# Optimization experiments

Hardware: AMD Instinct MI355X
Metric: run time of the kernel (lower is better)

## Reference

```python
import jax, jax.numpy as jnp
import numpy as np

GRAPH_SIZE = 100000  # == N, used as scalar multiplier on Q


def setup_inputs() -> dict:
    key = jax.random.key(0)
    ks = jax.random.split(key, 10)
    N, D, K, C, S = 100000, 128, 10, 50000, 100
    inp = {
        "seeds_idx_pad": jax.random.randint(ks[0], (1, S), 0, N + 1),  # N = pad row
        "seeds_idx_num": jnp.full((1, 1), 50.0, dtype=jnp.float32),
        "candidates_idx": jax.random.randint(ks[1], (C,), 0, N),
        "all_nodes": jnp.arange(N),
        "mask": jnp.ones((N, 1), dtype=jnp.float32),
        "features": jax.random.normal(ks[2], (N, D), dtype=jnp.float32),
        "neigh_idx": jax.random.randint(ks[3], (N, K), 0, N),
        "W_self": jax.random.normal(ks[4], (D, D), dtype=jnp.float32) * 0.05,
        "W_neigh": jax.random.normal(ks[5], (D, D), dtype=jnp.float32) * 0.05,
        "W1": jax.random.normal(ks[6], (D, D + 1), dtype=jnp.float32) * 0.05,
        "W2": jax.random.normal(ks[7], (D, D + 1), dtype=jnp.float32) * 0.05,
        "W3": jax.random.normal(ks[8], (D, D + 1), dtype=jnp.float32) * 0.05,
    }
    return inp


def _sage(features, neigh_idx, all_nodes, mask, W_self, W_neigh):
    x = features[all_nodes]                 # [N, D]
    nb_mean = features[neigh_idx].mean(axis=1)  # [N, K, D] -> [N, D]
    h = jax.nn.relu(x @ W_self + nb_mean @ W_neigh)
    return h * mask                          # [N, D]


def reference(seeds_idx_pad, seeds_idx_num, candidates_idx, all_nodes, mask,
              features, neigh_idx, W_self, W_neigh, W1, W2, W3):
    D = features.shape[1]
    embedding = _sage(features, neigh_idx, all_nodes, mask, W_self, W_neigh)  # [N, D]
    embedding_pad = jnp.concatenate([embedding, jnp.zeros((1, D), embedding.dtype)], axis=0)
    seeds_emb = embedding_pad[seeds_idx_pad]                  # [1, S, D]
    seeds_mean = jax.nn.sigmoid((seeds_emb.sum(axis=1) / seeds_idx_num) @ W1)  # [1, D+1]
    global_mean = jax.nn.sigmoid(embedding.mean(axis=0)[None, :] @ W2)         # computed but unused, as in source
    candi_emb = jax.nn.sigmoid(embedding[candidates_idx] @ W3)                 # [C, D+1]
    Q = (1.0 - jnp.sum(candi_emb * seeds_mean, axis=1)) * GRAPH_SIZE           # [C]
    return Q
```

## Files before the change

### kernel.cpp

```cpp
#include <hip/hip_runtime.h>

#define D     128
#define DP1   129
#define KN    10
#define GSZ   100000.0f

typedef __attribute__((ext_vector_type(8))) short bf16x8;
typedef __attribute__((ext_vector_type(4))) float f32x4;

#define MFMA16(a, b, c) __builtin_amdgcn_mfma_f32_16x16x32_bf16((a), (b), (c), 0, 0, 0)

__device__ __forceinline__ float sigmoidf_(float x) {
    return 1.0f / (1.0f + __expf(-x));
}
__device__ __forceinline__ unsigned short f2bf(float f) {
    unsigned u = __float_as_uint(f);
    u += 0x7FFFu + ((u >> 16) & 1u);
    return (unsigned short)(u >> 16);
}
__device__ __forceinline__ unsigned pack2bf(float lo, float hi) {
    return (unsigned)f2bf(lo) | ((unsigned)f2bf(hi) << 16);
}

__global__ __launch_bounds__(256) void prep_kernel(
    const float* __restrict__ features,
    const float* __restrict__ Wself, const float* __restrict__ Wneigh,
    const float* __restrict__ W3,
    const int*   __restrict__ seeds,
    const int*   __restrict__ all_nodes,
    const float* __restrict__ mask,
    const int*   __restrict__ neigh,
    unsigned short* __restrict__ featb,
    unsigned short* __restrict__ W2T,
    unsigned short* __restrict__ W3T,
    float*          __restrict__ srow,
    int N, int nFeatBlk, int doW)
{
    int b = blockIdx.x;
    const int t = threadIdx.x;

    if (b < nFeatBlk) {
        const int i = b * 256 + t;
        const int n8 = N * D / 8;
        if (i < n8) {
            const float4 a = *(const float4*)(features + (size_t)i * 8);
            const float4 c = *(const float4*)(features + (size_t)i * 8 + 4);
            bf16x8 v;
            v[0] = (short)f2bf(a.x); v[1] = (short)f2bf(a.y);
            v[2] = (short)f2bf(a.z); v[3] = (short)f2bf(a.w);
            v[4] = (short)f2bf(c.x); v[5] = (short)f2bf(c.y);
            v[6] = (short)f2bf(c.z); v[7] = (short)f2bf(c.w);
            *(bf16x8*)(featb + (size_t)i * 8) = v;
        }
        return;
    }
    b -= nFeatBlk;

    if (b < doW * 200) {
        const int u = b * 256 + t;
        if (u < 128 * 256) {
            int n = u >> 8, k = u & 255;
            float v = (k < 128) ? Wself[k * 128 + n] : Wneigh[(k - 128) * 128 + n];
            W2T[n * 256 + k] = f2bf(v);
        } else {
            int w = u - 128 * 256;
            if (w < 144 * 128) {
                int j = w >> 7, k = w & 127;
                float v = (j < DP1) ? W3[k * DP1 + j] : 0.0f;
                W3T[j * 128 + k] = f2bf(v);
            }
        }
        return;
    }
    b -= doW * 200;

    const int node = seeds[b];
    if (node >= N || node < 0) {
        if (t < D) srow[b * D + t] = 0.f;
        return;
    }
    __shared__ float xs[D], nb[D];
    if (t < D) {
        xs[t] = features[(size_t)all_nodes[node] * D + t];
        float a = 0.f;
        #pragma unroll
        for (int k = 0; k < KN; ++k)
            a += features[(size_t)neigh[node * KN + k] * D + t];
        nb[t] = a * (1.0f / KN);
    }
    __syncthreads();
    if (t < D) {
        float h = 0.f;
        #pragma unroll 4
        for (int dp = 0; dp < D; ++dp)
            h = fmaf(xs[dp], Wself[dp * D + t], fmaf(nb[dp], Wneigh[dp * D + t], h));
        srow[b * D + t] = fmaxf(h, 0.f) * mask[node];
    }
}

__global__ __launch_bounds__(256) void sm_kernel(
    const float* __restrict__ srow, int S,
    const float* __restrict__ snum,
    const float* __restrict__ W1,
    float*       __restrict__ smp)
{
    __shared__ float s[D];
    const int t = threadIdx.x;
    if (t < D) {
        float a = 0.f;
        for (int b = 0; b < S; ++b) a += srow[b * D + t];
        s[t] = a / snum[0];
    }
    __syncthreads();
    if (t < DP1) {
        float a = 0.f;
        #pragma unroll 4
        for (int dp = 0; dp < D; ++dp)
            a = fmaf(s[dp], W1[dp * DP1 + t], a);
        smp[t] = sigmoidf_(a);
    } else if (t < 144) {
        smp[t] = 0.0f;
    }
}

__global__ __launch_bounds__(256, 4) void fused_kernel(
    const int*            __restrict__ cand,
    const int*            __restrict__ all_nodes,
    const float*          __restrict__ mask,
    const unsigned short* __restrict__ featb,
    const int*            __restrict__ neigh,
    const unsigned short* __restrict__ W2T,
    const unsigned short* __restrict__ W3T,
    const float*          __restrict__ smp,
    float*                __restrict__ Q,
    int C)
{
    __shared__ unsigned short tile[16][256];

    const int lane  = threadIdx.x & 63;
    const int wv    = threadIdx.x >> 6;
    const int cbase = blockIdx.x * 16;

    #pragma unroll
    for (int r = 0; r < 4; ++r) {
        const int m  = wv * 4 + r;
        const int cc = cbase + m;
        const int nd = cand[(cc < C) ? cc : 0];
        const int fr = all_nodes[nd];

        const unsigned xv = *(const unsigned*)(featb + (size_t)fr * D + lane * 2);

        const int* nr = neigh + nd * KN;
        float ax = 0.f, ay = 0.f;
        #pragma unroll
        for (int k = 0; k < KN; ++k) {
            const unsigned v = *(const unsigned*)(featb + (size_t)nr[k] * D + lane * 2);
            ax += __uint_as_float((v & 0xFFFFu) << 16);
            ay += __uint_as_float(v & 0xFFFF0000u);
        }

        const int sw = (m & 7) << 3;
        *(unsigned*)(&tile[m][(lane * 2) ^ sw])       = xv;
        *(unsigned*)(&tile[m][(128 + lane * 2) ^ sw]) =
            pack2bf(ax * (1.0f / KN), ay * (1.0f / KN));
    }
    __syncthreads();
    if (wv != 0) return;

    const int g   = lane >> 4;
    const int n15 = lane & 15;
    const unsigned short* tp = &tile[0][0];
    const int swr = (n15 & 7) << 3;

    bf16x8 afr[8];
    #pragma unroll
    for (int ks = 0; ks < 8; ++ks)
        afr[ks] = *(const bf16x8*)(tp + n15 * 256 + ((ks * 32 + g * 8) ^ swr));

    f32x4 acc1[8];
    #pragma unroll
    for (int nt = 0; nt < 8; ++nt) acc1[nt] = (f32x4){0.f, 0.f, 0.f, 0.f};

    #pragma unroll
    for (int ks = 0; ks < 8; ++ks) {
        const unsigned short* bp = W2T + n15 * 256 + ks * 32 + g * 8;
        #pragma unroll
        for (int nt = 0; nt < 8; ++nt) {
            const bf16x8 bfr = *(const bf16x8*)(bp + nt * 16 * 256);
            acc1[nt] = MFMA16(afr[ks], bfr, acc1[nt]);
        }
    }

    float mrow[4];
    #pragma unroll
    for (int r = 0; r < 4; ++r) {
        const int cr = cbase + g * 4 + r;
        mrow[r] = (cr < C) ? mask[cand[cr]] : 0.f;
    }
    #pragma unroll
    for (int nt = 0; nt < 8; ++nt) {
        const f32x4 v = acc1[nt];
        #pragma unroll
        for (int r = 0; r < 4; ++r) {
            const int m2 = g * 4 + r;
            tile[m2][(nt * 16 + n15) ^ ((m2 & 7) << 3)] =
                f2bf(fmaxf(v[r], 0.f) * mrow[r]);
        }
    }

    bf16x8 ah[4];
    #pragma unroll
    for (int ks = 0; ks < 4; ++ks)
        ah[ks] = *(const bf16x8*)(tp + n15 * 256 + ((ks * 32 + g * 8) ^ swr));

    f32x4 acc2[9];
    #pragma unroll
    for (int jt = 0; jt < 9; ++jt) acc2[jt] = (f32x4){0.f, 0.f, 0.f, 0.f};

    #pragma unroll
    for (int ks = 0; ks < 4; ++ks) {
        const unsigned short* bp = W3T + n15 * 128 + ks * 32 + g * 8;
        #pragma unroll
        for (int jt = 0; jt < 9; ++jt) {
            const bf16x8 bfr = *(const bf16x8*)(bp + jt * 16 * 128);
            acc2[jt] = MFMA16(ah[ks], bfr, acc2[jt]);
        }
    }

    float qp[4] = {0.f, 0.f, 0.f, 0.f};
    #pragma unroll
    for (int jt = 0; jt < 9; ++jt) {
        const float smj = smp[jt * 16 + n15];
        const f32x4 v = acc2[jt];
        #pragma unroll
        for (int r = 0; r < 4; ++r)
            qp[r] += smj * sigmoidf_(v[r]);
    }
    #pragma unroll
    for (int off = 8; off >= 1; off >>= 1)
        #pragma unroll
        for (int r = 0; r < 4; ++r)
            qp[r] += __shfl_xor(qp[r], off);

    if (n15 == 0) {
        #pragma unroll
        for (int r = 0; r < 4; ++r) {
            const int cr = cbase + g * 4 + r;
            if (cr < C) Q[cr] = (1.0f - qp[r]) * GSZ;
        }
    }
}

#define MCAND 8
__global__ __launch_bounds__(128) void cand_kernel(
    const int*   __restrict__ cand,
    const int*   __restrict__ all_nodes,
    const float* __restrict__ mask,
    const float* __restrict__ features,
    const int*   __restrict__ neigh,
    const float* __restrict__ Wself,
    const float* __restrict__ Wneigh,
    const float* __restrict__ W3,
    const float* __restrict__ sm,
    float*       __restrict__ Q,
    int C)
{
    const int c0 = blockIdx.x * MCAND;
    const int t  = threadIdx.x;

    __shared__ float z[2 * MCAND][D];
    __shared__ float h[MCAND][D];
    __shared__ float red1[MCAND][D];
    __shared__ float red2[MCAND][D];
    __shared__ float smsh[DP1];

    smsh[t] = sm[t];
    if (t == 0) smsh[D] = sm[D];

    float msk[MCAND];
    #pragma unroll
    for (int m = 0; m < MCAND; ++m) {
        const int c    = c0 + m;
        const int node = (c < C) ? cand[c] : cand[0];
        msk[m] = mask[node];
        z[m][t] = features[(size_t)all_nodes[node] * D + t];
        float a = 0.f;
        #pragma unroll
        for (int k = 0; k < KN; ++k)
            a += features[(size_t)neigh[node * KN + k] * D + t];
        z[MCAND + m][t] = a * (1.0f / KN);
    }
    __syncthreads();

    float acc[MCAND];
    #pragma unroll
    for (int m = 0; m < MCAND; ++m) acc[m] = 0.f;
    for (int dp = 0; dp < D; dp += 4) {
        const float ws0 = Wself[(dp + 0) * D + t];
        const float ws1 = Wself[(dp + 1) * D + t];
        const float ws2 = Wself[(dp + 2) * D + t];
        const float ws3 = Wself[(dp + 3) * D + t];
        const float wn0 = Wneigh[(dp + 0) * D + t];
        const float wn1 = Wneigh[(dp + 1) * D + t];
        const float wn2 = Wneigh[(dp + 2) * D + t];
        const float wn3 = Wneigh[(dp + 3) * D + t];
        #pragma unroll
        for (int m = 0; m < MCAND; ++m) {
            const float4 xv = *(const float4*)&z[m][dp];
            const float4 nv = *(const float4*)&z[MCAND + m][dp];
            float a = acc[m];
            a = fmaf(xv.x, ws0, a); a = fmaf(xv.y, ws1, a);
            a = fmaf(xv.z, ws2, a); a = fmaf(xv.w, ws3, a);
            a = fmaf(nv.x, wn0, a); a = fmaf(nv.y, wn1, a);
            a = fmaf(nv.z, wn2, a); a = fmaf(nv.w, wn3, a);
            acc[m] = a;
        }
    }
    #pragma unroll
    for (int m = 0; m < MCAND; ++m)
        h[m][t] = fmaxf(acc[m], 0.f) * msk[m];
    __syncthreads();

    #pragma unroll
    for (int m = 0; m < MCAND; ++m) acc[m] = 0.f;
    for (int dp = 0; dp < D; dp += 4) {
        const float w0 = W3[(dp + 0) * DP1 + t];
        const float w1 = W3[(dp + 1) * DP1 + t];
        const float w2 = W3[(dp + 2) * DP1 + t];
        const float w3 = W3[(dp + 3) * DP1 + t];
        #pragma unroll
        for (int m = 0; m < MCAND; ++m) {
            const float4 hv = *(const float4*)&h[m][dp];
            float a = acc[m];
            a = fmaf(hv.x, w0, a); a = fmaf(hv.y, w1, a);
            a = fmaf(hv.z, w2, a); a = fmaf(hv.w, w3, a);
            acc[m] = a;
        }
    }

    const float w128 = W3[t * DP1 + D];
    const float smt  = smsh[t];
    #pragma unroll
    for (int m = 0; m < MCAND; ++m) {
        red1[m][t] = smt * sigmoidf_(acc[m]);
        red2[m][t] = h[m][t] * w128;
    }
    __syncthreads();

    for (int off = 64; off > 0; off >>= 1) {
        if (t < off) {
            #pragma unroll
            for (int m = 0; m < MCAND; ++m) {
                red1[m][t] += red1[m][t + off];
                red2[m][t] += red2[m][t + off];
            }
        }
        __syncthreads();
    }

    if (t < MCAND && (c0 + t) < C) {
        const float dot = red1[t][0] + smsh[D] * sigmoidf_(red2[t][0]);
        Q[c0 + t] = (1.0f - dot) * GSZ;
    }
}

extern "C" void kernel_launch(void* const* d_in, const int* in_sizes, int n_in,
                              void* d_out, int out_size, void* d_ws, size_t ws_size,
                              hipStream_t stream)
{
    const int*   seeds    = (const int*)  d_in[0];
    const float* snum     = (const float*)d_in[1];
    const int*   cand     = (const int*)  d_in[2];
    const int*   allnodes = (const int*)  d_in[3];
    const float* mask     = (const float*)d_in[4];
    const float* features = (const float*)d_in[5];
    const int*   neigh    = (const int*)  d_in[6];
    const float* Wself    = (const float*)d_in[7];
    const float* Wneigh   = (const float*)d_in[8];
    const float* W1       = (const float*)d_in[9];
    const float* W3       = (const float*)d_in[11];

    float* Q = (float*)d_out;

    const int S = in_sizes[0];
    const int C = in_sizes[2];
    const int N = in_sizes[3];

    char* ws = (char*)d_ws;
    float*          srow  = (float*)ws;
    float*          smp   = (float*)(ws + 57344);
    unsigned short* W2T   = (unsigned short*)(ws + 65536);
    unsigned short* W3T   = (unsigned short*)(ws + 131072);
    unsigned short* featb = (unsigned short*)(ws + 167936);
    const size_t need = 167936 + (size_t)N * D * 2;
    const bool small_ok = (size_t)S * D * 4 <= 57344;

    if (ws_size >= need && small_ok && (N * D % 2048) == 0) {
        const int nFeatBlk = N * D / 2048;
        prep_kernel<<<nFeatBlk + 200 + S, 256, 0, stream>>>(
            features, Wself, Wneigh, W3, seeds, allnodes, mask, neigh,
            featb, W2T, W3T, srow, N, nFeatBlk, 1);
        sm_kernel<<<1, 256, 0, stream>>>(srow, S, snum, W1, smp);
        const int nTiles = (C + 15) / 16;
        fused_kernel<<<nTiles, 256, 0, stream>>>(cand, allnodes, mask, featb,
                                                 neigh, W2T, W3T, smp, Q, C);
    } else {
        prep_kernel<<<S, 256, 0, stream>>>(
            features, Wself, Wneigh, W3, seeds, allnodes, mask, neigh,
            (unsigned short*)ws, (unsigned short*)ws, (unsigned short*)ws,
            srow, N, 0, 0);
        sm_kernel<<<1, 256, 0, stream>>>(srow, S, snum, W1, smp);
        const int nblk = (C + MCAND - 1) / MCAND;
        cand_kernel<<<nblk, 128, 0, stream>>>(cand, allnodes, mask, features,
                                              neigh, Wself, Wneigh, W3, smp, Q, C);
    }
}
```

Before: 108.8 us.

## Split MFMA work across all four waves and widen gather loads

The fused kernel now spreads both matmul stages over all four waves: each wave computes two N-tiles of the first GEMM and two or three output tiles of the second, with partial Q sums reduced through shared memory. Previously only wave 0 did the MFMA work after the gather. The neighbour gather also moves to 16-byte loads, with 16 lanes per candidate row, and the first W2T fragments are prefetched before the barrier. The seed-mean kernel splits its row reduction across two thread halves. These changes add extra barriers and shared-memory reductions, and the launch-bounds occupancy hint is dropped.

```diff
diff --git a/kernel.cpp b/kernel.cpp
--- a/kernel.cpp
+++ b/kernel.cpp
@@ -7,6 +7,7 @@
 
 typedef __attribute__((ext_vector_type(8))) short bf16x8;
 typedef __attribute__((ext_vector_type(4))) float f32x4;
+typedef __attribute__((ext_vector_type(4))) unsigned uintx4;
 
 #define MFMA16(a, b, c) __builtin_amdgcn_mfma_f32_16x16x32_bf16((a), (b), (c), 0, 0, 0)
 
@@ -104,26 +105,29 @@
     const float* __restrict__ W1,
     float*       __restrict__ smp)
 {
+    __shared__ float ps[2][D];
     __shared__ float s[D];
-    const int t = threadIdx.x;
-    if (t < D) {
-        float a = 0.f;
-        for (int b = 0; b < S; ++b) a += srow[b * D + t];
-        s[t] = a / snum[0];
-    }
+    const int t   = threadIdx.x;
+    const int col = t & 127;
+    const int hf  = t >> 7;
+    float a = 0.f;
+    for (int b = hf; b < S; b += 2) a += srow[b * D + col];
+    ps[hf][col] = a;
+    __syncthreads();
+    if (t < D) s[t] = (ps[0][t] + ps[1][t]) / snum[0];
     __syncthreads();
     if (t < DP1) {
-        float a = 0.f;
+        float acc = 0.f;
         #pragma unroll 4
         for (int dp = 0; dp < D; ++dp)
-            a = fmaf(s[dp], W1[dp * DP1 + t], a);
-        smp[t] = sigmoidf_(a);
+            acc = fmaf(s[dp], W1[dp * DP1 + t], acc);
+        smp[t] = sigmoidf_(acc);
     } else if (t < 144) {
         smp[t] = 0.0f;
     }
 }
 
-__global__ __launch_bounds__(256, 4) void fused_kernel(
+__global__ __launch_bounds__(256) void fused_kernel(
     const int*            __restrict__ cand,
     const int*            __restrict__ all_nodes,
     const float*          __restrict__ mask,
@@ -136,105 +140,138 @@
     int C)
 {
     __shared__ unsigned short tile[16][256];
+    __shared__ float msk[16];
+    __shared__ float qred[4][16];
 
     const int lane  = threadIdx.x & 63;
     const int wv    = threadIdx.x >> 6;
     const int cbase = blockIdx.x * 16;
 
-    #pragma unroll
-    for (int r = 0; r < 4; ++r) {
-        const int m  = wv * 4 + r;
-        const int cc = cbase + m;
-        const int nd = cand[(cc < C) ? cc : 0];
-        const int fr = all_nodes[nd];
-
-        const unsigned xv = *(const unsigned*)(featb + (size_t)fr * D + lane * 2);
-
-        const int* nr = neigh + nd * KN;
-        float ax = 0.f, ay = 0.f;
+    const int L   = lane & 15;
+    const int grp = lane >> 4;
+    const int m   = wv * 4 + grp;
+
+    {
+        const int cc  = cbase + m;
+        const int nd  = cand[(cc < C) ? cc : 0];
+        const int fr  = all_nodes[nd];
+        if (L == 0) msk[m] = (cc < C) ? mask[nd] : 0.f;
+
+        int rix[KN];
+        #pragma unroll
+        for (int k = 0; k < KN; ++k) rix[k] = neigh[nd * KN + k];
+
+        const uintx4 xv = *(const uintx4*)(featb + (size_t)fr * D + L * 8);
+
+        float a8[8];
+        #pragma unroll
+        for (int i = 0; i < 8; ++i) a8[i] = 0.f;
+
         #pragma unroll
         for (int k = 0; k < KN; ++k) {
-            const unsigned v = *(const unsigned*)(featb + (size_t)nr[k] * D + lane * 2);
-            ax += __uint_as_float((v & 0xFFFFu) << 16);
-            ay += __uint_as_float(v & 0xFFFF0000u);
+            const uintx4 v = *(const uintx4*)(featb + (size_t)rix[k] * D + L * 8);
+            #pragma unroll
+            for (int i = 0; i < 4; ++i) {
+                a8[2 * i]     += __uint_as_float(v[i] << 16);
+                a8[2 * i + 1] += __uint_as_float(v[i] & 0xFFFF0000u);
+            }
         }
 
         const int sw = (m & 7) << 3;
-        *(unsigned*)(&tile[m][(lane * 2) ^ sw])       = xv;
-        *(unsigned*)(&tile[m][(128 + lane * 2) ^ sw]) =
-            pack2bf(ax * (1.0f / KN), ay * (1.0f / KN));
-    }
-    __syncthreads();
-    if (wv != 0) return;
+        unsigned short* tp = &tile[0][0];
+        *(uintx4*)(tp + m * 256 + ((L * 8) ^ sw)) = xv;
+        uintx4 nb;
+        #pragma unroll
+        for (int i = 0; i < 4; ++i)
+            nb[i] = pack2bf(a8[2 * i] * (1.0f / KN), a8[2 * i + 1] * (1.0f / KN));
+        *(uintx4*)(tp + m * 256 + ((128 + L * 8) ^ sw)) = nb;
+    }
 
     const int g   = lane >> 4;
     const int n15 = lane & 15;
+    const int swr = (n15 & 7) << 3;
     const unsigned short* tp = &tile[0][0];
-    const int swr = (n15 & 7) << 3;
+
+    bf16x8 bq0 = *(const bf16x8*)(W2T + ((wv * 2 + 0) * 16 + n15) * 256 + g * 8);
+    bf16x8 bq1 = *(const bf16x8*)(W2T + ((wv * 2 + 1) * 16 + n15) * 256 + g * 8);
+
+    __syncthreads();
 
     bf16x8 afr[8];
     #pragma unroll
     for (int ks = 0; ks < 8; ++ks)
         afr[ks] = *(const bf16x8*)(tp + n15 * 256 + ((ks * 32 + g * 8) ^ swr));
 
-    f32x4 acc1[8];
-    #pragma unroll
-    for (int nt = 0; nt < 8; ++nt) acc1[nt] = (f32x4){0.f, 0.f, 0.f, 0.f};
-
-    #pragma unroll
-    for (int ks = 0; ks < 8; ++ks) {
-        const unsigned short* bp = W2T + n15 * 256 + ks * 32 + g * 8;
-        #pragma unroll
-        for (int nt = 0; nt < 8; ++nt) {
-            const bf16x8 bfr = *(const bf16x8*)(bp + nt * 16 * 256);
-            acc1[nt] = MFMA16(afr[ks], bfr, acc1[nt]);
-        }
-    }
-
-    float mrow[4];
-    #pragma unroll
-    for (int r = 0; r < 4; ++r) {
-        const int cr = cbase + g * 4 + r;
-        mrow[r] = (cr < C) ? mask[cand[cr]] : 0.f;
-    }
-    #pragma unroll
-    for (int nt = 0; nt < 8; ++nt) {
-        const f32x4 v = acc1[nt];
+    f32x4 acc1[2];
+    acc1[0] = (f32x4){0.f, 0.f, 0.f, 0.f};
+    acc1[1] = (f32x4){0.f, 0.f, 0.f, 0.f};
+
+    acc1[0] = MFMA16(afr[0], bq0, acc1[0]);
+    acc1[1] = MFMA16(afr[0], bq1, acc1[1]);
+    #pragma unroll
+    for (int ks = 1; ks < 8; ++ks) {
+        #pragma unroll
+        for (int i = 0; i < 2; ++i) {
+            const bf16x8 b = *(const bf16x8*)(W2T + ((wv * 2 + i) * 16 + n15) * 256
+                                              + ks * 32 + g * 8);
+            acc1[i] = MFMA16(afr[ks], b, acc1[i]);
+        }
+    }
+
+    float mr[4];
+    #pragma unroll
+    for (int r = 0; r < 4; ++r) mr[r] = msk[g * 4 + r];
+
+    #pragma unroll
+    for (int i = 0; i < 2; ++i) {
+        const f32x4 v = acc1[i];
         #pragma unroll
         for (int r = 0; r < 4; ++r) {
             const int m2 = g * 4 + r;
-            tile[m2][(nt * 16 + n15) ^ ((m2 & 7) << 3)] =
-                f2bf(fmaxf(v[r], 0.f) * mrow[r]);
-        }
-    }
+            tile[m2][(((wv * 2 + i) * 16 + n15)) ^ ((m2 & 7) << 3)] =
+                f2bf(fmaxf(v[r], 0.f) * mr[r]);
+        }
+    }
+    __syncthreads();
 
     bf16x8 ah[4];
     #pragma unroll
     for (int ks = 0; ks < 4; ++ks)
         ah[ks] = *(const bf16x8*)(tp + n15 * 256 + ((ks * 32 + g * 8) ^ swr));
 
-    f32x4 acc2[9];
-    #pragma unroll
-    for (int jt = 0; jt < 9; ++jt) acc2[jt] = (f32x4){0.f, 0.f, 0.f, 0.f};
+    const int jt0 = wv, jt1 = 4 + wv;
+    f32x4 acc2[3];
+    acc2[0] = (f32x4){0.f, 0.f, 0.f, 0.f};
+    acc2[1] = (f32x4){0.f, 0.f, 0.f, 0.f};
+    acc2[2] = (f32x4){0.f, 0.f, 0.f, 0.f};
 
     #pragma unroll
     for (int ks = 0; ks < 4; ++ks) {
-        const unsigned short* bp = W3T + n15 * 128 + ks * 32 + g * 8;
-        #pragma unroll
-        for (int jt = 0; jt < 9; ++jt) {
-            const bf16x8 bfr = *(const bf16x8*)(bp + jt * 16 * 128);
-            acc2[jt] = MFMA16(ah[ks], bfr, acc2[jt]);
+        const bf16x8 b0 = *(const bf16x8*)(W3T + (jt0 * 16 + n15) * 128 + ks * 32 + g * 8);
+        acc2[0] = MFMA16(ah[ks], b0, acc2[0]);
+        const bf16x8 b1 = *(const bf16x8*)(W3T + (jt1 * 16 + n15) * 128 + ks * 32 + g * 8);
+        acc2[1] = MFMA16(ah[ks], b1, acc2[1]);
+        if (wv == 0) {
+            const bf16x8 b2 = *(const bf16x8*)(W3T + (8 * 16 + n15) * 128 + ks * 32 + g * 8);
+            acc2[2] = MFMA16(ah[ks], b2, acc2[2]);
         }
     }
 
     float qp[4] = {0.f, 0.f, 0.f, 0.f};
-    #pragma unroll
-    for (int jt = 0; jt < 9; ++jt) {
-        const float smj = smp[jt * 16 + n15];
-        const f32x4 v = acc2[jt];
-        #pragma unroll
-        for (int r = 0; r < 4; ++r)
-            qp[r] += smj * sigmoidf_(v[r]);
+    {
+        const float sm0 = smp[jt0 * 16 + n15];
+        const float sm1 = smp[jt1 * 16 + n15];
+        #pragma unroll
+        for (int r = 0; r < 4; ++r) {
+            qp[r] += sm0 * sigmoidf_(acc2[0][r]);
+            qp[r] += sm1 * sigmoidf_(acc2[1][r]);
+        }
+        if (wv == 0) {
+            const float sm2 = smp[8 * 16 + n15];
+            #pragma unroll
+            for (int r = 0; r < 4; ++r)
+                qp[r] += sm2 * sigmoidf_(acc2[2][r]);
+        }
     }
     #pragma unroll
     for (int off = 8; off >= 1; off >>= 1)
@@ -244,10 +281,16 @@
 
     if (n15 == 0) {
         #pragma unroll
-        for (int r = 0; r < 4; ++r) {
-            const int cr = cbase + g * 4 + r;
-            if (cr < C) Q[cr] = (1.0f - qp[r]) * GSZ;
-        }
+        for (int r = 0; r < 4; ++r)
+            qred[wv][g * 4 + r] = qp[r];
+    }
+    __syncthreads();
+
+    const int t = threadIdx.x;
+    if (t < 16) {
+        const float s = qred[0][t] + qred[1][t] + qred[2][t] + qred[3][t];
+        const int cr = cbase + t;
+        if (cr < C) Q[cr] = (1.0f - s) * GSZ;
     }
 }
 
@@ -277,12 +320,12 @@
     smsh[t] = sm[t];
     if (t == 0) smsh[D] = sm[D];
 
-    float msk[MCAND];
+    float mskv[MCAND];
     #pragma unroll
     for (int m = 0; m < MCAND; ++m) {
         const int c    = c0 + m;
         const int node = (c < C) ? cand[c] : cand[0];
-        msk[m] = mask[node];
+        mskv[m] = mask[node];
         z[m][t] = features[(size_t)all_nodes[node] * D + t];
         float a = 0.f;
         #pragma unroll
@@ -318,7 +361,7 @@
     }
     #pragma unroll
     for (int m = 0; m < MCAND; ++m)
-        h[m][t] = fmaxf(acc[m], 0.f) * msk[m];
+        h[m][t] = fmaxf(acc[m], 0.f) * mskv[m];
     __syncthreads();
 
     #pragma unroll
```

Result: faster. 96.19 us (-11.6%).
